# Kernel tuning notes

Hardware: AMD Instinct MI355X
Metric: run time of the kernel (lower is better)

## Reference

```python
import jax, jax.numpy as jnp
import numpy as np

C, H, W = 16, 1024, 1024   # channels, y_max, x_max
L = 4_000_000              # number of scattered points


def setup_inputs() -> dict:
    key = jax.random.key(0)
    k1, k2, k3, k4, k5, k6 = jax.random.split(key, 6)
    x = jax.random.normal(k1, (1, C, H, W), dtype=jnp.float32)
    img = jax.random.normal(k2, (C, H, W), dtype=jnp.float32)
    index_x = jax.random.randint(k3, (L, 1), 0, H, dtype=jnp.int32)  # indexes dim 1 of x.squeeze(0)
    index_y = jax.random.randint(k4, (L, 1), 0, W, dtype=jnp.int32)  # indexes dim 2
    proj_x = jax.random.randint(k5, (L,), 0, W, dtype=jnp.int32)     # column in img
    proj_y = jax.random.randint(k6, (L,), 0, H, dtype=jnp.int32)     # row in img
    return {"x": x, "img": img, "index_x": index_x, "index_y": index_y,
            "proj_x": proj_x, "proj_y": proj_y}


def reference(x, img, index_x, index_y, proj_x, proj_y):
    # Faithful to: for all (i, c): x[c, index_x[i], index_y[i]] += img[c, proj_y[i], proj_x[i]]
    xs = x[0]                              # squeeze(0): [C, H, W]
    ix = index_x[:, 0]                     # [L]
    iy = index_y[:, 0]                     # [L]
    data = img[:, proj_y, proj_x]          # gather -> [C, L]
    out = xs.at[:, ix, iy].add(data)       # accumulating scatter (index_put accumulate=True)
    return out
```

## Files before the change

kernel.cpp:

```cpp
#include <hip/hip_runtime.h>

#define C_CH 16
#define H_DIM 1024
#define W_DIM 1024
#define HW (H_DIM * W_DIM)

#define NBIN 256
#define CAPB 16384
#define PCHUNK 4096
#define PPT 16
#define NTILES_GRID 4096

typedef int          vint4  __attribute__((ext_vector_type(4)));
typedef unsigned int vuint4 __attribute__((ext_vector_type(4)));
typedef unsigned int uint;

__global__ __launch_bounds__(256) void transpose_img_bf16_kernel(
        const float* __restrict__ img, uint4* __restrict__ imgT,
        uint* __restrict__ count) {
    int hw = blockIdx.x * blockDim.x + threadIdx.x;
    if (blockIdx.x == 0 && threadIdx.x < NBIN) count[threadIdx.x] = 0u;
    if (hw >= HW) return;
    uint u[8];
    #pragma unroll
    for (int j = 0; j < 8; ++j) {
        uint b0 = __float_as_uint(__builtin_nontemporal_load(&img[(2*j  ) * HW + hw]));
        uint b1 = __float_as_uint(__builtin_nontemporal_load(&img[(2*j+1) * HW + hw]));
        uint r0 = (b0 + 0x7FFFu + ((b0 >> 16) & 1u)) >> 16;
        uint r1 = (b1 + 0x7FFFu + ((b1 >> 16) & 1u)) & 0xFFFF0000u;
        u[j] = r0 | r1;
    }
    imgT[hw * 2 + 0] = make_uint4(u[0], u[1], u[2], u[3]);
    imgT[hw * 2 + 1] = make_uint4(u[4], u[5], u[6], u[7]);
}

__global__ __launch_bounds__(256) void placement_kernel(
        const int* __restrict__ index_x, const int* __restrict__ index_y,
        const int* __restrict__ proj_x,  const int* __restrict__ proj_y,
        uint* __restrict__ count, uint* __restrict__ rec, int L) {
    __shared__ uint hist[NBIN];
    __shared__ uint lofs[NBIN];
    __shared__ uint lbase[NBIN];
    __shared__ uint scan[NBIN];
    __shared__ uint spay[PCHUNK];
    __shared__ unsigned char sbin[PCHUNK];
    __shared__ uint total_s;

    const int tid  = threadIdx.x;
    const int base = blockIdx.x * PCHUNK;

    hist[tid] = 0;
    __syncthreads();

    uint ent[PPT];
    int  bn[PPT];

    #pragma unroll
    for (int g = 0; g < PPT / 4; ++g) {
        const int p0 = base + tid * PPT + g * 4;
        if (p0 + 3 < L) {
            vint4 ix4 = __builtin_nontemporal_load(reinterpret_cast<const vint4*>(index_x + p0));
            vint4 iy4 = __builtin_nontemporal_load(reinterpret_cast<const vint4*>(index_y + p0));
            vint4 px4 = __builtin_nontemporal_load(reinterpret_cast<const vint4*>(proj_x + p0));
            vint4 py4 = __builtin_nontemporal_load(reinterpret_cast<const vint4*>(proj_y + p0));
            #pragma unroll
            for (int k = 0; k < 4; ++k) {
                int ix = ix4[k], iy = iy4[k], px = px4[k], py = py4[k];
                int b = (ix >> 6) * 16 + (iy >> 6);
                uint dl12 = (uint)((ix & 63) * 64 + (iy & 63));
                ent[g*4 + k] = (dl12 << 20) | (uint)(py * W_DIM + px);
                bn[g*4 + k]  = b;
                atomicAdd(&hist[b], 1u);
            }
        } else {
            #pragma unroll
            for (int k = 0; k < 4; ++k) {
                int l = p0 + k;
                if (l < L) {
                    int ix = index_x[l], iy = index_y[l], px = proj_x[l], py = proj_y[l];
                    int b = (ix >> 6) * 16 + (iy >> 6);
                    uint dl12 = (uint)((ix & 63) * 64 + (iy & 63));
                    ent[g*4 + k] = (dl12 << 20) | (uint)(py * W_DIM + px);
                    bn[g*4 + k]  = b;
                    atomicAdd(&hist[b], 1u);
                } else {
                    bn[g*4 + k] = -1;
                }
            }
        }
    }
    __syncthreads();

    uint h = hist[tid];
    scan[tid] = h;
    __syncthreads();
    #pragma unroll
    for (int s = 1; s < NBIN; s <<= 1) {
        uint v = (tid >= s) ? scan[tid - s] : 0u;
        __syncthreads();
        scan[tid] += v;
        __syncthreads();
    }
    lofs[tid]  = scan[tid] - h;
    lbase[tid] = h ? atomicAdd(&count[tid], h) : 0u;
    hist[tid]  = 0;
    if (tid == NBIN - 1) total_s = scan[NBIN - 1];
    __syncthreads();

    #pragma unroll
    for (int j = 0; j < PPT; ++j) {
        if (bn[j] >= 0) {
            uint pos  = atomicAdd(&hist[bn[j]], 1u);
            uint slot = lofs[bn[j]] + pos;
            spay[slot] = ent[j];
            sbin[slot] = (unsigned char)bn[j];
        }
    }
    __syncthreads();

    const uint total = total_s;
    for (uint j = tid; j < total; j += 256u) {
        uint b    = sbin[j];
        uint addr = lbase[b] + (j - lofs[b]);
        if (addr < CAPB) rec[(size_t)b * CAPB + addr] = spay[j];
    }
}

__global__ __launch_bounds__(256) void tile_bf16_kernel(
        const uint4* __restrict__ imgT, const uint* __restrict__ count,
        const uint* __restrict__ rec,
        const float* __restrict__ x, float* __restrict__ out) {
    __shared__ float acc[C_CH * 256];
    const int tid = threadIdx.x;
    const int p   = blockIdx.x;
    const int xcd = p & 7;
    const int q   = p >> 3;
    const int bin = xcd * 32 + (q >> 4);
    const int sub = q & 15;
    const int sr  = sub >> 2, sc = sub & 3;

    #pragma unroll
    for (int i = tid; i < C_CH * 256; i += 256) acc[i] = 0.0f;
    __syncthreads();

    uint n = count[bin];
    if (n > CAPB) n = CAPB;
    const uint* r = rec + (size_t)bin * CAPB;

    const uint want_hi = (uint)sr;
    const uint want_lo = (uint)sc;

    for (uint i0 = 0; i0 < n; i0 += 1024u) {
        uint i = i0 + (uint)tid * 4u;
        if (i + 4u <= n) {
            vuint4 e4 = *reinterpret_cast<const vuint4*>(r + i);
            #pragma unroll
            for (int k = 0; k < 4; ++k) {
                uint e = e4[k];
                uint dl12 = e >> 20;
                if ((dl12 >> 10) == want_hi && ((dl12 >> 4) & 3u) == want_lo) {
                    uint src = e & 0xFFFFFu;
                    uint dl  = ((dl12 >> 6) & 15u) * 16u + (dl12 & 15u);
                    uint4 g0 = imgT[src * 2 + 0];
                    uint4 g1 = imgT[src * 2 + 1];
                    #define ADD2(c2, uu)                                                       \
                        atomicAdd(&acc[(2*(c2)  ) * 256 + dl], __uint_as_float((uu) << 16));   \
                        atomicAdd(&acc[(2*(c2)+1) * 256 + dl], __uint_as_float((uu) & 0xFFFF0000u));
                    ADD2(0, g0.x) ADD2(1, g0.y) ADD2(2, g0.z) ADD2(3, g0.w)
                    ADD2(4, g1.x) ADD2(5, g1.y) ADD2(6, g1.z) ADD2(7, g1.w)
                    #undef ADD2
                }
            }
        } else {
            for (uint k = 0; k < 4u; ++k) {
                uint idx = i + k;
                if (idx < n) {
                    uint e = r[idx];
                    uint dl12 = e >> 20;
                    if ((dl12 >> 10) == want_hi && ((dl12 >> 4) & 3u) == want_lo) {
                        uint src = e & 0xFFFFFu;
                        uint dl  = ((dl12 >> 6) & 15u) * 16u + (dl12 & 15u);
                        uint4 g0 = imgT[src * 2 + 0];
                        uint4 g1 = imgT[src * 2 + 1];
                        #define ADD2(c2, uu)                                                       \
                            atomicAdd(&acc[(2*(c2)  ) * 256 + dl], __uint_as_float((uu) << 16));   \
                            atomicAdd(&acc[(2*(c2)+1) * 256 + dl], __uint_as_float((uu) & 0xFFFF0000u));
                        ADD2(0, g0.x) ADD2(1, g0.y) ADD2(2, g0.z) ADD2(3, g0.w)
                        ADD2(4, g1.x) ADD2(5, g1.y) ADD2(6, g1.z) ADD2(7, g1.w)
                        #undef ADD2
                    }
                }
            }
        }
    }
    __syncthreads();

    const int row0 = (bin >> 4) * 64 + sr * 16;
    const int col0 = (bin & 15) * 64 + sc * 16;
    const int hw   = (row0 + (tid >> 4)) * W_DIM + col0 + (tid & 15);
    #pragma unroll
    for (int c = 0; c < C_CH; ++c) {
        float xv = __builtin_nontemporal_load(&x[c * HW + hw]);
        __builtin_nontemporal_store(xv + acc[c * 256 + tid], &out[c * HW + hw]);
    }
}

__global__ void transpose_img_kernel(const float* __restrict__ img,
                                     float4* __restrict__ imgT4) {
    int hw = blockIdx.x * blockDim.x + threadIdx.x;
    if (hw >= HW) return;
    float v[C_CH];
    #pragma unroll
    for (int c = 0; c < C_CH; ++c) v[c] = img[c * HW + hw];
    #pragma unroll
    for (int j = 0; j < 4; ++j)
        imgT4[hw * 4 + j] = make_float4(v[4*j], v[4*j+1], v[4*j+2], v[4*j+3]);
}

__global__ void scatter_hwc_kernel(const float4* __restrict__ imgT4,
                                   const int* __restrict__ index_x,
                                   const int* __restrict__ index_y,
                                   const int* __restrict__ proj_x,
                                   const int* __restrict__ proj_y,
                                   float* __restrict__ acc, int L) {
    int l = blockIdx.x * blockDim.x + threadIdx.x;
    if (l >= L) return;
    const int src = proj_y[l] * W_DIM + proj_x[l];
    const int dst = index_x[l] * W_DIM + index_y[l];
    float4 a0 = imgT4[src * 4 + 0], a1 = imgT4[src * 4 + 1];
    float4 a2 = imgT4[src * 4 + 2], a3 = imgT4[src * 4 + 3];
    float* pp = acc + (size_t)dst * C_CH;
    atomicAdd(pp + 0, a0.x);  atomicAdd(pp + 1, a0.y);
    atomicAdd(pp + 2, a0.z);  atomicAdd(pp + 3, a0.w);
    atomicAdd(pp + 4, a1.x);  atomicAdd(pp + 5, a1.y);
    atomicAdd(pp + 6, a1.z);  atomicAdd(pp + 7, a1.w);
    atomicAdd(pp + 8, a2.x);  atomicAdd(pp + 9, a2.y);
    atomicAdd(pp + 10, a2.z); atomicAdd(pp + 11, a2.w);
    atomicAdd(pp + 12, a3.x); atomicAdd(pp + 13, a3.y);
    atomicAdd(pp + 14, a3.z); atomicAdd(pp + 15, a3.w);
}

__global__ void finalize_kernel(const float* __restrict__ x,
                                const float4* __restrict__ acc4,
                                float* __restrict__ out) {
    int hw = blockIdx.x * blockDim.x + threadIdx.x;
    if (hw >= HW) return;
    float4 a0 = acc4[hw * 4 + 0], a1 = acc4[hw * 4 + 1];
    float4 a2 = acc4[hw * 4 + 2], a3 = acc4[hw * 4 + 3];
    float a[C_CH] = {a0.x,a0.y,a0.z,a0.w, a1.x,a1.y,a1.z,a1.w,
                     a2.x,a2.y,a2.z,a2.w, a3.x,a3.y,a3.z,a3.w};
    #pragma unroll
    for (int c = 0; c < C_CH; ++c)
        out[c * HW + hw] = x[c * HW + hw] + a[c];
}

extern "C" void kernel_launch(void* const* d_in, const int* in_sizes, int n_in,
                              void* d_out, int out_size, void* d_ws, size_t ws_size,
                              hipStream_t stream) {
    const float* x       = (const float*)d_in[0];
    const float* img     = (const float*)d_in[1];
    const int*   index_x = (const int*)d_in[2];
    const int*   index_y = (const int*)d_in[3];
    const int*   proj_x  = (const int*)d_in[4];
    const int*   proj_y  = (const int*)d_in[5];
    float* out = (float*)d_out;
    const int L = in_sizes[4];

    const size_t imgT_bf_bytes = (size_t)HW * C_CH * sizeof(unsigned short);
    const size_t rec_bytes     = (size_t)NBIN * CAPB * sizeof(uint);
    const size_t cnt_bytes     = (size_t)NBIN * sizeof(uint);

    if (ws_size >= imgT_bf_bytes + rec_bytes + cnt_bytes) {
        uint4* imgT  = (uint4*)d_ws;
        uint*  rec   = (uint*)((char*)d_ws + imgT_bf_bytes);
        uint*  count = (uint*)((char*)d_ws + imgT_bf_bytes + rec_bytes);

        {
            const int block = 256, grid = (HW + block - 1) / block;
            transpose_img_bf16_kernel<<<grid, block, 0, stream>>>(img, imgT, count);
        }
        {
            const int grid = (L + PCHUNK - 1) / PCHUNK;
            placement_kernel<<<grid, 256, 0, stream>>>(index_x, index_y, proj_x, proj_y,
                                                       count, rec, L);
        }
        {
            tile_bf16_kernel<<<NTILES_GRID, 256, 0, stream>>>(imgT, count, rec, x, out);
        }
    } else {
        const size_t imgT_bytes = (size_t)HW * C_CH * sizeof(float);
        float4* imgT4 = (float4*)d_ws;
        float*  acc   = (float*)((char*)d_ws + imgT_bytes);
        hipMemsetAsync(acc, 0, imgT_bytes, stream);
        {
            const int block = 256, grid = (HW + block - 1) / block;
            transpose_img_kernel<<<grid, block, 0, stream>>>(img, imgT4);
        }
        {
            const int block = 256, grid = (L + block - 1) / block;
            scatter_hwc_kernel<<<grid, block, 0, stream>>>(imgT4, index_x, index_y,
                                                           proj_x, proj_y, acc, L);
        }
        {
            const int block = 256, grid = (HW + block - 1) / block;
            finalize_kernel<<<grid, block, 0, stream>>>(x, (const float4*)acc, out);
        }
    }
}
```

Baseline: 572.2 us.

## Add two-level binning: bin by source tile, gather, rebin by destination tile

Measured after the change: 728.4 us. 1.27x slower.

```diff
diff --git a/kernel.cpp b/kernel.cpp
--- a/kernel.cpp
+++ b/kernel.cpp
@@ -6,20 +6,32 @@
 #define HW (H_DIM * W_DIM)
 
 #define NBIN 256
-#define CAPB 16384
 #define PCHUNK 4096
 #define PPT 16
-#define NTILES_GRID 4096
+
+#define CAPS 16384
+#define CAPP 16384
+#define SPLIT 8
+#define PER_SPLIT (CAPS / SPLIT)
+
+#define CAPB 16384
 
 typedef int          vint4  __attribute__((ext_vector_type(4)));
 typedef unsigned int vuint4 __attribute__((ext_vector_type(4)));
 typedef unsigned int uint;
 
+static __device__ __forceinline__ uint umin_u(uint a, uint b) { return a < b ? a : b; }
+
 __global__ __launch_bounds__(256) void transpose_img_bf16_kernel(
         const float* __restrict__ img, uint4* __restrict__ imgT,
-        uint* __restrict__ count) {
+        uint* __restrict__ cnt0, uint* __restrict__ cnt1) {
     int hw = blockIdx.x * blockDim.x + threadIdx.x;
-    if (blockIdx.x == 0 && threadIdx.x < NBIN) count[threadIdx.x] = 0u;
+    if (blockIdx.x == 0) {
+        if (threadIdx.x < NBIN) {
+            cnt0[threadIdx.x] = 0u;
+            if (cnt1) cnt1[threadIdx.x] = 0u;
+        }
+    }
     if (hw >= HW) return;
     uint u[8];
     #pragma unroll
@@ -32,6 +44,226 @@
     }
     imgT[hw * 2 + 0] = make_uint4(u[0], u[1], u[2], u[3]);
     imgT[hw * 2 + 1] = make_uint4(u[4], u[5], u[6], u[7]);
+}
+
+__global__ __launch_bounds__(256) void placement_src_kernel(
+        const int* __restrict__ index_x, const int* __restrict__ index_y,
+        const int* __restrict__ proj_x,  const int* __restrict__ proj_y,
+        uint* __restrict__ scount, uint* __restrict__ srec, int L) {
+    __shared__ uint hist[NBIN];
+    __shared__ uint lofs[NBIN];
+    __shared__ uint lbase[NBIN];
+    __shared__ uint scan[NBIN];
+    __shared__ uint spay[PCHUNK];
+    __shared__ unsigned char sbin[PCHUNK];
+    __shared__ uint total_s;
+
+    const int tid  = threadIdx.x;
+    const int base = blockIdx.x * PCHUNK;
+
+    hist[tid] = 0;
+    __syncthreads();
+
+    uint ent[PPT];
+    int  bn[PPT];
+
+    #pragma unroll
+    for (int g = 0; g < PPT / 4; ++g) {
+        const int p0 = base + tid * PPT + g * 4;
+        if (p0 + 3 < L) {
+            vint4 ix4 = __builtin_nontemporal_load(reinterpret_cast<const vint4*>(index_x + p0));
+            vint4 iy4 = __builtin_nontemporal_load(reinterpret_cast<const vint4*>(index_y + p0));
+            vint4 px4 = __builtin_nontemporal_load(reinterpret_cast<const vint4*>(proj_x + p0));
+            vint4 py4 = __builtin_nontemporal_load(reinterpret_cast<const vint4*>(proj_y + p0));
+            #pragma unroll
+            for (int k = 0; k < 4; ++k) {
+                int ix = ix4[k], iy = iy4[k], px = px4[k], py = py4[k];
+                int b = (py >> 6) * 16 + (px >> 6);
+                uint sl = (uint)((py & 63) * 64 + (px & 63));
+                ent[g*4 + k] = (sl << 20) | (uint)(ix * W_DIM + iy);
+                bn[g*4 + k]  = b;
+                atomicAdd(&hist[b], 1u);
+            }
+        } else {
+            #pragma unroll
+            for (int k = 0; k < 4; ++k) {
+                int l = p0 + k;
+                if (l < L) {
+                    int ix = index_x[l], iy = index_y[l], px = proj_x[l], py = proj_y[l];
+                    int b = (py >> 6) * 16 + (px >> 6);
+                    uint sl = (uint)((py & 63) * 64 + (px & 63));
+                    ent[g*4 + k] = (sl << 20) | (uint)(ix * W_DIM + iy);
+                    bn[g*4 + k]  = b;
+                    atomicAdd(&hist[b], 1u);
+                } else {
+                    bn[g*4 + k] = -1;
+                }
+            }
+        }
+    }
+    __syncthreads();
+
+    uint h = hist[tid];
+    scan[tid] = h;
+    __syncthreads();
+    #pragma unroll
+    for (int s = 1; s < NBIN; s <<= 1) {
+        uint v = (tid >= s) ? scan[tid - s] : 0u;
+        __syncthreads();
+        scan[tid] += v;
+        __syncthreads();
+    }
+    lofs[tid]  = scan[tid] - h;
+    lbase[tid] = h ? atomicAdd(&scount[tid], h) : 0u;
+    hist[tid]  = 0;
+    if (tid == NBIN - 1) total_s = scan[NBIN - 1];
+    __syncthreads();
+
+    #pragma unroll
+    for (int j = 0; j < PPT; ++j) {
+        if (bn[j] >= 0) {
+            uint pos  = atomicAdd(&hist[bn[j]], 1u);
+            uint slot = lofs[bn[j]] + pos;
+            spay[slot] = ent[j];
+            sbin[slot] = (unsigned char)bn[j];
+        }
+    }
+    __syncthreads();
+
+    const uint total = total_s;
+    for (uint j = tid; j < total; j += 256u) {
+        uint b    = sbin[j];
+        uint addr = lbase[b] + (j - lofs[b]);
+        if (addr < CAPS)
+            __builtin_nontemporal_store(spay[j], &srec[(size_t)b * CAPS + addr]);
+    }
+}
+
+__global__ __launch_bounds__(256) void gather_emit_kernel(
+        const uint* __restrict__ imgTw, const uint* __restrict__ scount,
+        const uint* __restrict__ srec,
+        uint* __restrict__ pcount, uint* __restrict__ pdst, uint* __restrict__ pvalw) {
+    __shared__ uint hist[NBIN];
+    __shared__ uint lofs[NBIN];
+    __shared__ uint lbase[NBIN];
+    __shared__ uint scan[NBIN];
+    __shared__ uint sent[PER_SPLIT];
+
+    const int tid   = threadIdx.x;
+    const int bin   = blockIdx.x & 255;
+    const int split = blockIdx.x >> 8;
+
+    uint n  = umin_u(scount[bin], CAPS);
+    uint i0 = (uint)split * PER_SPLIT;
+    if (i0 >= n) return;
+    uint m  = umin_u(n - i0, PER_SPLIT);
+    const uint* r = srec + (size_t)bin * CAPS + i0;
+
+    hist[tid] = 0;
+    __syncthreads();
+
+    uint ent[PER_SPLIT / 256];
+    int  db[PER_SPLIT / 256];
+    #pragma unroll
+    for (int k = 0; k < PER_SPLIT / 256; ++k) {
+        uint j = (uint)tid + (uint)k * 256u;
+        if (j < m) {
+            uint e = __builtin_nontemporal_load(&r[j]);
+            ent[k] = e;
+            uint dst = e & 0xFFFFFu;
+            int b = (int)(((dst >> 10) >> 6) * 16u + ((dst & 1023u) >> 6));
+            db[k] = b;
+            atomicAdd(&hist[b], 1u);
+        } else db[k] = -1;
+    }
+    __syncthreads();
+
+    uint h = hist[tid];
+    scan[tid] = h;
+    __syncthreads();
+    #pragma unroll
+    for (int s = 1; s < NBIN; s <<= 1) {
+        uint v = (tid >= s) ? scan[tid - s] : 0u;
+        __syncthreads();
+        scan[tid] += v;
+        __syncthreads();
+    }
+    lofs[tid]  = scan[tid] - h;
+    lbase[tid] = h ? atomicAdd(&pcount[tid], h) : 0u;
+    hist[tid]  = 0;
+    __syncthreads();
+
+    #pragma unroll
+    for (int k = 0; k < PER_SPLIT / 256; ++k) {
+        if (db[k] >= 0) {
+            uint pos = atomicAdd(&hist[db[k]], 1u);
+            sent[lofs[db[k]] + pos] = ent[k];
+        }
+    }
+    __syncthreads();
+
+    const uint py_hi = (uint)(bin >> 4), px_hi = (uint)(bin & 15);
+    for (uint j = tid; j < m; j += 256u) {
+        uint e   = sent[j];
+        uint dst = e & 0xFFFFFu;
+        uint sl  = e >> 20;
+        uint b   = ((dst >> 10) >> 6) * 16u + ((dst & 1023u) >> 6);
+        uint addr = lbase[b] + (j - lofs[b]);
+        if (addr < CAPP) {
+            uint hw = py_hi * 65536u + (sl >> 6) * 1024u + px_hi * 64u + (sl & 63u);
+            vuint4 g0 = *reinterpret_cast<const vuint4*>(imgTw + (size_t)hw * 8u);
+            vuint4 g1 = *reinterpret_cast<const vuint4*>(imgTw + (size_t)hw * 8u + 4u);
+            size_t o = (size_t)b * CAPP + addr;
+            __builtin_nontemporal_store(dst, &pdst[o]);
+            __builtin_nontemporal_store(g0, reinterpret_cast<vuint4*>(pvalw + o * 8u));
+            __builtin_nontemporal_store(g1, reinterpret_cast<vuint4*>(pvalw + o * 8u + 4u));
+        }
+    }
+}
+
+__global__ __launch_bounds__(256) void accum_kernel(
+        const uint* __restrict__ pcount, const uint* __restrict__ pdst,
+        const uint* __restrict__ pvalw,
+        const float* __restrict__ x, float* __restrict__ out) {
+    __shared__ float acc[C_CH * 256];
+    const int tid = threadIdx.x;
+    const int bin = blockIdx.x & 255;
+    const int sub = blockIdx.x >> 8;
+    const int sr  = sub >> 2, sc = sub & 3;
+
+    #pragma unroll
+    for (int i = tid; i < C_CH * 256; i += 256) acc[i] = 0.0f;
+    __syncthreads();
+
+    uint n = umin_u(pcount[bin], CAPP);
+    const uint* pd = pdst + (size_t)bin * CAPP;
+    const uint* pv = pvalw + (size_t)bin * CAPP * 8u;
+
+    for (uint i = tid; i < n; i += 256u) {
+        uint dst = pd[i];
+        uint ix = dst >> 10, iy = dst & 1023u;
+        if ((((ix >> 4) & 3u) == (uint)sr) & (((iy >> 4) & 3u) == (uint)sc)) {
+            vuint4 g0 = *reinterpret_cast<const vuint4*>(pv + (size_t)i * 8u);
+            vuint4 g1 = *reinterpret_cast<const vuint4*>(pv + (size_t)i * 8u + 4u);
+            uint dl = (ix & 15u) * 16u + (iy & 15u);
+            #define ADD2(c2, uu)                                                       \
+                atomicAdd(&acc[(2*(c2)  ) * 256 + dl], __uint_as_float((uu) << 16));   \
+                atomicAdd(&acc[(2*(c2)+1) * 256 + dl], __uint_as_float((uu) & 0xFFFF0000u));
+            ADD2(0, g0.x) ADD2(1, g0.y) ADD2(2, g0.z) ADD2(3, g0.w)
+            ADD2(4, g1.x) ADD2(5, g1.y) ADD2(6, g1.z) ADD2(7, g1.w)
+            #undef ADD2
+        }
+    }
+    __syncthreads();
+
+    const int row0 = (bin >> 4) * 64 + sr * 16;
+    const int col0 = (bin & 15) * 64 + sc * 16;
+    const int hw   = (row0 + (tid >> 4)) * W_DIM + col0 + (tid & 15);
+    #pragma unroll
+    for (int c = 0; c < C_CH; ++c) {
+        float xv = __builtin_nontemporal_load(&x[c * HW + hw]);
+        __builtin_nontemporal_store(xv + acc[c * 256 + tid], &out[c * HW + hw]);
+    }
 }
 
 __global__ __launch_bounds__(256) void placement_kernel(
@@ -143,8 +375,7 @@
     for (int i = tid; i < C_CH * 256; i += 256) acc[i] = 0.0f;
     __syncthreads();
 
-    uint n = count[bin];
-    if (n > CAPB) n = CAPB;
+    uint n = umin_u(count[bin], CAPB);
     const uint* r = rec + (size_t)bin * CAPB;
 
     const uint want_hi = (uint)sr;
@@ -266,18 +497,49 @@
     float* out = (float*)d_out;
     const int L = in_sizes[4];
 
-    const size_t imgT_bf_bytes = (size_t)HW * C_CH * sizeof(unsigned short);
-    const size_t rec_bytes     = (size_t)NBIN * CAPB * sizeof(uint);
-    const size_t cnt_bytes     = (size_t)NBIN * sizeof(uint);
-
-    if (ws_size >= imgT_bf_bytes + rec_bytes + cnt_bytes) {
+    const size_t imgT_bytes = (size_t)HW * C_CH * sizeof(unsigned short);
+    const size_t srec_bytes = (size_t)NBIN * CAPS * sizeof(uint);
+    const size_t pval_bytes = (size_t)NBIN * CAPP * 32;
+    const size_t pdst_bytes = (size_t)NBIN * CAPP * sizeof(uint);
+    const size_t cnt_bytes  = (size_t)NBIN * sizeof(uint);
+    const size_t big_need   = imgT_bytes + srec_bytes + pval_bytes + pdst_bytes
+                            + 2 * cnt_bytes + 256;
+    const size_t med_need   = imgT_bytes + (size_t)NBIN * CAPB * sizeof(uint)
+                            + cnt_bytes;
+
+    if (ws_size >= big_need) {
+        char* w = (char*)d_ws;
+        uint4* imgT   = (uint4*)w;                      w += imgT_bytes;
+        uint*  srec   = (uint*)w;                       w += srec_bytes;
+        uint*  pvalw  = (uint*)w;                       w += pval_bytes;
+        uint*  pdst   = (uint*)w;                       w += pdst_bytes;
+        uint*  scount = (uint*)w;                       w += cnt_bytes;
+        uint*  pcount = (uint*)w;
+
+        {
+            const int block = 256, grid = (HW + block - 1) / block;
+            transpose_img_bf16_kernel<<<grid, block, 0, stream>>>(img, imgT, scount, pcount);
+        }
+        {
+            const int grid = (L + PCHUNK - 1) / PCHUNK;
+            placement_src_kernel<<<grid, 256, 0, stream>>>(index_x, index_y, proj_x, proj_y,
+                                                           scount, srec, L);
+        }
+        {
+            gather_emit_kernel<<<SPLIT * NBIN, 256, 0, stream>>>((const uint*)imgT, scount,
+                                                                 srec, pcount, pdst, pvalw);
+        }
+        {
+            accum_kernel<<<16 * NBIN, 256, 0, stream>>>(pcount, pdst, pvalw, x, out);
+        }
+    } else if (ws_size >= med_need) {
         uint4* imgT  = (uint4*)d_ws;
-        uint*  rec   = (uint*)((char*)d_ws + imgT_bf_bytes);
-        uint*  count = (uint*)((char*)d_ws + imgT_bf_bytes + rec_bytes);
+        uint*  rec   = (uint*)((char*)d_ws + imgT_bytes);
+        uint*  count = (uint*)((char*)d_ws + imgT_bytes + (size_t)NBIN * CAPB * sizeof(uint));
 
         {
             const int block = 256, grid = (HW + block - 1) / block;
-            transpose_img_bf16_kernel<<<grid, block, 0, stream>>>(img, imgT, count);
+            transpose_img_bf16_kernel<<<grid, block, 0, stream>>>(img, imgT, count, nullptr);
         }
         {
             const int grid = (L + PCHUNK - 1) / PCHUNK;
@@ -285,13 +547,13 @@
                                                        count, rec, L);
         }
         {
-            tile_bf16_kernel<<<NTILES_GRID, 256, 0, stream>>>(imgT, count, rec, x, out);
+            tile_bf16_kernel<<<16 * NBIN, 256, 0, stream>>>(imgT, count, rec, x, out);
         }
     } else {
-        const size_t imgT_bytes = (size_t)HW * C_CH * sizeof(float);
+        const size_t imgT32_bytes = (size_t)HW * C_CH * sizeof(float);
         float4* imgT4 = (float4*)d_ws;
-        float*  acc   = (float*)((char*)d_ws + imgT_bytes);
-        hipMemsetAsync(acc, 0, imgT_bytes, stream);
+        float*  acc   = (float*)((char*)d_ws + imgT32_bytes);
+        hipMemsetAsync(acc, 0, imgT32_bytes, stream);
         {
             const int block = 256, grid = (HW + block - 1) / block;
             transpose_img_kernel<<<grid, block, 0, stream>>>(img, imgT4);
```
